# Kernel optimization log

Measured on AMD Instinct MI355X. Metric: run time of the kernel, lower is better.

## Reference

```python
import jax, jax.numpy as jnp
import numpy as np

NEG = -1e6  # masked_softmax fill value from the original code


def setup_inputs() -> dict:
    key = jax.random.key(0)
    ks = jax.random.split(key, 8)
    B, Q, K, Dq, Dk, Dv, H = 8, 256, 1024, 256, 256, 128, 128
    queries = jax.random.normal(ks[0], (B, Q, Dq), dtype=jnp.float32)
    keys = jax.random.normal(ks[1], (B, K, Dk), dtype=jnp.float32)
    values = jax.random.normal(ks[2], (B, K, Dv), dtype=jnp.float32)
    valid_lens = jax.random.randint(ks[3], (B,), 1, K + 1, dtype=jnp.int32)
    # learned params (Dense, use_bias=False): y = x @ W
    W_q = jax.random.normal(ks[4], (Dq, H), dtype=jnp.float32) / np.sqrt(Dq)
    W_k = jax.random.normal(ks[5], (Dk, H), dtype=jnp.float32) / np.sqrt(Dk)
    w_v = jax.random.normal(ks[6], (H,), dtype=jnp.float32) / np.sqrt(H)
    return {"queries": queries, "keys": keys, "values": values,
            "valid_lens": valid_lens, "W_q": W_q, "W_k": W_k, "w_v": w_v}


def reference(queries, keys, values, valid_lens, W_q, W_k, w_v):
    q = jnp.einsum('bqd,dh->bqh', queries, W_q)          # [B,Q,H]
    k = jnp.einsum('bkd,dh->bkh', keys, W_k)             # [B,K,H]
    features = jnp.tanh(q[:, :, None, :] + k[:, None, :, :])  # [B,Q,K,H]
    scores = jnp.einsum('bqkh,h->bqk', features, w_v)    # [B,Q,K]
    # masked softmax over last axis: positions >= valid_len set to -1e6
    K_len = scores.shape[-1]
    mask = jnp.arange(K_len)[None, None, :] < valid_lens[:, None, None]
    scores = jnp.where(mask, scores, NEG)
    attn = jax.nn.softmax(scores, axis=-1)
    return jnp.einsum('bqk,bkv->bqv', attn, values)      # [B,Q,Dv]
```

## Files before the change

kernel.cpp:

```cpp
#include <hip/hip_runtime.h>
#include <hip/hip_bf16.h>

#if defined(__has_builtin)
#if __has_builtin(__builtin_amdgcn_exp2f)
#define EXP2F __builtin_amdgcn_exp2f
#endif
#if __has_builtin(__builtin_amdgcn_rcpf)
#define RCPF __builtin_amdgcn_rcpf
#endif
#endif
#ifndef EXP2F
#define EXP2F exp2f
#endif
#ifndef RCPF
#define RCPF(x) (1.0f / (x))
#endif

#define B_  8
#define Q_  256
#define K_  1024
#define D_  256
#define H_  128
#define DV_ 128

#define CSL 2.8853900817779268f
#define L2E 1.4426950408889634f

#define QE_OFF   0
#define KE_OFF   262144
#define WPK_OFF  1310720
#define AVP_OFF  1310976
#define SP_OFF   1835264

__global__ __launch_bounds__(256) void proj_kernel(
    const float* __restrict__ queries, const float* __restrict__ keys,
    const float* __restrict__ Wq, const float* __restrict__ Wk,
    const float* __restrict__ w_v,
    float* __restrict__ qE, float2* __restrict__ kET2, float* __restrict__ wpk)
{
    __shared__ __align__(16) float As[64][68];
    __shared__ __align__(16) float Ws[64][64];

    const int tid = threadIdx.x;
    const int blk = blockIdx.x;
    const bool isQ = blk < 64;
    const int t = isQ ? blk : (blk - 64);
    const int rowtile = t >> 1;
    const int cbase = (t & 1) * 64;
    const int row0 = rowtile * 64;
    const float* A = isQ ? (queries + row0 * D_) : (keys + row0 * D_);
    const float* W = isQ ? Wq : Wk;

    float acc[4][4];
#pragma unroll
    for (int i = 0; i < 4; i++)
#pragma unroll
        for (int j = 0; j < 4; j++) acc[i][j] = 0.f;

    const int lr  = tid & 63;
    const int ldb = (tid >> 6) * 16;
    const int r4  = (tid >> 4) * 4;
    const int c4  = (tid & 15) * 4;

    for (int d0 = 0; d0 < D_; d0 += 64) {
#pragma unroll
        for (int j = 0; j < 4; j++) {
            const float4 a = *(const float4*)&A[lr * D_ + d0 + ldb + j * 4];
            As[ldb + j * 4 + 0][lr] = a.x;
            As[ldb + j * 4 + 1][lr] = a.y;
            As[ldb + j * 4 + 2][lr] = a.z;
            As[ldb + j * 4 + 3][lr] = a.w;
        }
#pragma unroll
        for (int l = 0; l < 4; l++) {
            const int idx = tid + l * 256;
            const int rr = idx >> 4, cc = (idx & 15) * 4;
            *(float4*)&Ws[rr][cc] = *(const float4*)&W[(d0 + rr) * H_ + cbase + cc];
        }
        __syncthreads();
#pragma unroll 4
        for (int d = 0; d < 64; d++) {
            const float4 a4 = *(const float4*)&As[d][r4];
            const float4 w4 = *(const float4*)&Ws[d][c4];
            const float ar[4] = {a4.x, a4.y, a4.z, a4.w};
#pragma unroll
            for (int i = 0; i < 4; i++) {
                acc[i][0] = fmaf(ar[i], w4.x, acc[i][0]);
                acc[i][1] = fmaf(ar[i], w4.y, acc[i][1]);
                acc[i][2] = fmaf(ar[i], w4.z, acc[i][2]);
                acc[i][3] = fmaf(ar[i], w4.w, acc[i][3]);
            }
        }
        __syncthreads();
    }

#pragma unroll
    for (int i = 0; i < 4; i++) {
        float e[4];
#pragma unroll
        for (int j = 0; j < 4; j++) e[j] = EXP2F(CSL * acc[i][j]);
        const int row = row0 + r4 + i;
        if (isQ) {
            *(float4*)&qE[row * H_ + cbase + c4] = make_float4(e[0], e[1], e[2], e[3]);
        } else {
            const int b = row >> 10, k = row & 1023;
            const int p0 = (cbase + c4) >> 1;
            kET2[(size_t)(b * 64 + p0) * K_ + k]     = make_float2(e[0], e[1]);
            kET2[(size_t)(b * 64 + p0 + 1) * K_ + k] = make_float2(e[2], e[3]);
        }
    }

    if (blk == 0 && tid < 64) {
        const float w1 = -2.0f * L2E * w_v[2 * tid];
        const float w2 = -2.0f * L2E * w_v[2 * tid + 1];
        *(float4*)&wpk[tid * 4] = make_float4(w1, w2, w1 + w2, 0.f);
    }
}

__global__ __launch_bounds__(512, 4) void attn_kernel(
    const float* __restrict__ qE,
    const float2* __restrict__ kET2,
    const float* __restrict__ values,
    const int*   __restrict__ valid_lens,
    const float* __restrict__ wpk,
    float* __restrict__ avpart,
    float* __restrict__ spart)
{
    __shared__ __align__(16) float sc[512][8];
    __shared__ __align__(16) float red[4][8][128];
    __shared__ __align__(16) float psum[8][8];

    const int tid = threadIdx.x;
    const int raw = blockIdx.x;
    const int kh  = raw >> 8;
    const int j   = raw & 255;
    const int b   = (j + kh) & 7;
    const int qt  = j >> 3;
    const int q0  = qt * 8;
    const int vl  = valid_lens[b];
    const int k   = kh * 512 + tid;

    const float* qp = qE + (b * Q_ + q0) * H_;

    float acc[8];
#pragma unroll
    for (int q = 0; q < 8; q++) acc[q] = 0.f;

    if (k < vl) {
        const float2* kb = kET2 + (size_t)(b * 64) * K_ + k;
#pragma unroll 2
        for (int p = 0; p < 64; p++) {
            const float2 ek = kb[(size_t)p * K_];
            const float4 wp = *(const float4*)&wpk[p * 4];
#pragma unroll
            for (int q = 0; q < 8; q++) {
                const float2 qq = *(const float2*)&qp[q * H_ + 2 * p];
                const float x1 = qq.x * ek.x, x2 = qq.y * ek.y;
                const float e1 = x1 + 1.f;
                const float d  = fmaf(e1, x2, e1);
                float n = fmaf(wp.y, x1, wp.z);
                n = fmaf(wp.x, x2, n);
                acc[q] = fmaf(n, RCPF(d), acc[q]);
            }
        }
    }

    const bool valid = k < vl;
    float p8[8];
#pragma unroll
    for (int q = 0; q < 8; q++) p8[q] = valid ? EXP2F(acc[q]) : 0.f;
    *(float4*)&sc[tid][0] = make_float4(p8[0], p8[1], p8[2], p8[3]);
    *(float4*)&sc[tid][4] = make_float4(p8[4], p8[5], p8[6], p8[7]);

    float s8[8];
#pragma unroll
    for (int q = 0; q < 8; q++) s8[q] = p8[q];
#pragma unroll
    for (int sh = 32; sh > 0; sh >>= 1) {
#pragma unroll
        for (int q = 0; q < 8; q++) s8[q] += __shfl_xor(s8[q], sh);
    }
    const int lane = tid & 63, w = tid >> 6;
    if (lane == 0) {
        *(float4*)&psum[w][0] = make_float4(s8[0], s8[1], s8[2], s8[3]);
        *(float4*)&psum[w][4] = make_float4(s8[4], s8[5], s8[6], s8[7]);
    }
    __syncthreads();
    if (tid < 8) {
        float t = 0.f;
#pragma unroll
        for (int ww = 0; ww < 8; ww++) t += psum[ww][tid];
        spart[kh * 2048 + b * Q_ + q0 + tid] = t;
    }

    const int v4  = tid & 31;
    const int qp2 = (tid >> 5) & 3;
    const int ks  = tid >> 7;
    const float* vb = values + (size_t)b * (K_ * DV_) + v4 * 4;
    float av[2][4];
#pragma unroll
    for (int qq = 0; qq < 2; qq++)
#pragma unroll
        for (int jj = 0; jj < 4; jj++) av[qq][jj] = 0.f;

    const int kbase = kh * 512 + ks * 128;
    const int rem = vl - kbase;
    const int imax = rem <= 0 ? 0 : (rem > 128 ? 128 : rem);
#pragma unroll 2
    for (int i = 0; i < imax; i++) {
        const int kl = ks * 128 + i;
        const float4 vv = *(const float4*)&vb[(kbase + i) * DV_];
        const float2 pp = *(const float2*)&sc[kl][2 * qp2];
        av[0][0] = fmaf(pp.x, vv.x, av[0][0]); av[0][1] = fmaf(pp.x, vv.y, av[0][1]);
        av[0][2] = fmaf(pp.x, vv.z, av[0][2]); av[0][3] = fmaf(pp.x, vv.w, av[0][3]);
        av[1][0] = fmaf(pp.y, vv.x, av[1][0]); av[1][1] = fmaf(pp.y, vv.y, av[1][1]);
        av[1][2] = fmaf(pp.y, vv.z, av[1][2]); av[1][3] = fmaf(pp.y, vv.w, av[1][3]);
    }
    *(float4*)&red[ks][2 * qp2][v4 * 4]     = make_float4(av[0][0], av[0][1], av[0][2], av[0][3]);
    *(float4*)&red[ks][2 * qp2 + 1][v4 * 4] = make_float4(av[1][0], av[1][1], av[1][2], av[1][3]);
    __syncthreads();

    if (tid < 256) {
        const int q = tid >> 5, vv4 = tid & 31;
        float4 t = make_float4(0.f, 0.f, 0.f, 0.f);
#pragma unroll
        for (int g = 0; g < 4; g++) {
            const float4 r = *(const float4*)&red[g][q][vv4 * 4];
            t.x += r.x; t.y += r.y; t.z += r.z; t.w += r.w;
        }
        *(float4*)&avpart[(size_t)(kh * 2048 + b * Q_ + q0 + q) * DV_ + vv4 * 4] = t;
    }
}

__global__ __launch_bounds__(256) void combine_kernel(
    const float* __restrict__ avpart, const float* __restrict__ spart,
    float* __restrict__ out)
{
    const int idx = (blockIdx.x * 256 + threadIdx.x) * 4;
    const int row = idx >> 7;
    const float4 a0 = *(const float4*)&avpart[idx];
    const float4 a1 = *(const float4*)&avpart[2048 * DV_ + idx];
    const float r = RCPF(spart[row] + spart[2048 + row]);
    *(float4*)&out[idx] = make_float4((a0.x + a1.x) * r, (a0.y + a1.y) * r,
                                      (a0.z + a1.z) * r, (a0.w + a1.w) * r);
}

extern "C" void kernel_launch(void* const* d_in, const int* in_sizes, int n_in,
                              void* d_out, int out_size, void* d_ws, size_t ws_size,
                              hipStream_t stream) {
    const float* queries    = (const float*)d_in[0];
    const float* keys       = (const float*)d_in[1];
    const float* values     = (const float*)d_in[2];
    const int*   valid_lens = (const int*)d_in[3];
    const float* W_q        = (const float*)d_in[4];
    const float* W_k        = (const float*)d_in[5];
    const float* w_v        = (const float*)d_in[6];
    float* out = (float*)d_out;

    float*  ws     = (float*)d_ws;
    float*  qE     = ws + QE_OFF;
    float2* kET2   = (float2*)(ws + KE_OFF);
    float*  wpk    = ws + WPK_OFF;
    float*  avpart = ws + AVP_OFF;
    float*  spart  = ws + SP_OFF;

    proj_kernel<<<320, 256, 0, stream>>>(queries, keys, W_q, W_k, w_v, qE, kET2, wpk);
    attn_kernel<<<512, 512, 0, stream>>>(qE, kET2, values, valid_lens, wpk, avpart, spart);
    combine_kernel<<<256, 256, 0, stream>>>(avpart, spart, out);
}
```

Baseline: 143.5 us.

## Split attention into 128-key chunks with early exit past valid length

The attention kernel is restructured from 512 blocks of 512 threads (two K halves, 8 queries) into 2048 blocks of 256 threads, each handling 8 queries over a 128-key chunk. Whole chunks beyond valid_len now exit immediately, which skips wasted work on padded keys and lets the grid balance across CUs with more, smaller blocks. The in-block AV reduction through shared memory is removed. In exchange the combine kernel sums up to 8 partials per row, and the partial buffers grow, so spart is moved to a new workspace offset.

```diff
diff --git a/kernel.cpp b/kernel.cpp
--- a/kernel.cpp
+++ b/kernel.cpp
@@ -30,7 +30,7 @@
 #define KE_OFF   262144
 #define WPK_OFF  1310720
 #define AVP_OFF  1310976
-#define SP_OFF   1835264
+#define SP_OFF   3408128
 
 __global__ __launch_bounds__(256) void proj_kernel(
     const float* __restrict__ queries, const float* __restrict__ keys,
@@ -117,7 +117,7 @@
     }
 }
 
-__global__ __launch_bounds__(512, 4) void attn_kernel(
+__global__ __launch_bounds__(256, 8) void attn_kernel(
     const float* __restrict__ qE,
     const float2* __restrict__ kET2,
     const float* __restrict__ values,
@@ -126,25 +126,25 @@
     float* __restrict__ avpart,
     float* __restrict__ spart)
 {
-    __shared__ __align__(16) float sc[512][8];
-    __shared__ __align__(16) float red[4][8][128];
-    __shared__ __align__(16) float psum[8][8];
+    __shared__ float sc[8][128];
+    __shared__ __align__(16) float psum[4][4];
 
     const int tid = threadIdx.x;
-    const int raw = blockIdx.x;
-    const int kh  = raw >> 8;
-    const int j   = raw & 255;
-    const int b   = (j + kh) & 7;
-    const int qt  = j >> 3;
-    const int q0  = qt * 8;
-    const int vl  = valid_lens[b];
-    const int k   = kh * 512 + tid;
-
-    const float* qp = qE + (b * Q_ + q0) * H_;
-
-    float acc[8];
-#pragma unroll
-    for (int q = 0; q < 8; q++) acc[q] = 0.f;
+    const int idx = blockIdx.x;
+    const int b  = idx & 7;
+    const int ks = (idx >> 3) & 7;
+    const int qt = idx >> 6;
+    const int vl = valid_lens[b];
+    const int k0 = ks * 128;
+    if (k0 >= vl) return;
+
+    const int q0 = qt * 8;
+    const int kl = tid & 127;
+    const int qh = tid >> 7;
+    const int k  = k0 + kl;
+    const float* qp = qE + (b * Q_ + q0 + qh * 4) * H_;
+
+    float acc[4] = {0.f, 0.f, 0.f, 0.f};
 
     if (k < vl) {
         const float2* kb = kET2 + (size_t)(b * 64) * K_ + k;
@@ -153,7 +153,7 @@
             const float2 ek = kb[(size_t)p * K_];
             const float4 wp = *(const float4*)&wpk[p * 4];
 #pragma unroll
-            for (int q = 0; q < 8; q++) {
+            for (int q = 0; q < 4; q++) {
                 const float2 qq = *(const float2*)&qp[q * H_ + 2 * p];
                 const float x1 = qq.x * ek.x, x2 = qq.y * ek.y;
                 const float e1 = x1 + 1.f;
@@ -166,83 +166,64 @@
     }
 
     const bool valid = k < vl;
-    float p8[8];
-#pragma unroll
-    for (int q = 0; q < 8; q++) p8[q] = valid ? EXP2F(acc[q]) : 0.f;
-    *(float4*)&sc[tid][0] = make_float4(p8[0], p8[1], p8[2], p8[3]);
-    *(float4*)&sc[tid][4] = make_float4(p8[4], p8[5], p8[6], p8[7]);
-
-    float s8[8];
-#pragma unroll
-    for (int q = 0; q < 8; q++) s8[q] = p8[q];
+    float p4[4];
+#pragma unroll
+    for (int q = 0; q < 4; q++) {
+        p4[q] = valid ? EXP2F(acc[q]) : 0.f;
+        sc[qh * 4 + q][kl] = p4[q];
+    }
 #pragma unroll
     for (int sh = 32; sh > 0; sh >>= 1) {
 #pragma unroll
-        for (int q = 0; q < 8; q++) s8[q] += __shfl_xor(s8[q], sh);
+        for (int q = 0; q < 4; q++) p4[q] += __shfl_xor(p4[q], sh);
     }
     const int lane = tid & 63, w = tid >> 6;
-    if (lane == 0) {
-        *(float4*)&psum[w][0] = make_float4(s8[0], s8[1], s8[2], s8[3]);
-        *(float4*)&psum[w][4] = make_float4(s8[4], s8[5], s8[6], s8[7]);
-    }
+    if (lane == 0) *(float4*)&psum[w][0] = make_float4(p4[0], p4[1], p4[2], p4[3]);
     __syncthreads();
     if (tid < 8) {
-        float t = 0.f;
-#pragma unroll
-        for (int ww = 0; ww < 8; ww++) t += psum[ww][tid];
-        spart[kh * 2048 + b * Q_ + q0 + tid] = t;
-    }
-
-    const int v4  = tid & 31;
-    const int qp2 = (tid >> 5) & 3;
-    const int ks  = tid >> 7;
-    const float* vb = values + (size_t)b * (K_ * DV_) + v4 * 4;
-    float av[2][4];
-#pragma unroll
-    for (int qq = 0; qq < 2; qq++)
-#pragma unroll
-        for (int jj = 0; jj < 4; jj++) av[qq][jj] = 0.f;
-
-    const int kbase = kh * 512 + ks * 128;
-    const int rem = vl - kbase;
-    const int imax = rem <= 0 ? 0 : (rem > 128 ? 128 : rem);
+        const int qh2 = tid >> 2, j = tid & 3;
+        spart[ks * 2048 + b * Q_ + q0 + tid] =
+            psum[2 * qh2][j] + psum[2 * qh2 + 1][j];
+    }
+
+    const int v4 = (tid & 31) * 4;
+    const int q  = tid >> 5;
+    const float* vb = values + (size_t)b * (K_ * DV_) + (size_t)k0 * DV_ + v4;
+    float av0 = 0.f, av1 = 0.f, av2 = 0.f, av3 = 0.f;
+    const int rem = vl - k0;
+    const int imax = rem > 128 ? 128 : rem;
 #pragma unroll 2
     for (int i = 0; i < imax; i++) {
-        const int kl = ks * 128 + i;
-        const float4 vv = *(const float4*)&vb[(kbase + i) * DV_];
-        const float2 pp = *(const float2*)&sc[kl][2 * qp2];
-        av[0][0] = fmaf(pp.x, vv.x, av[0][0]); av[0][1] = fmaf(pp.x, vv.y, av[0][1]);
-        av[0][2] = fmaf(pp.x, vv.z, av[0][2]); av[0][3] = fmaf(pp.x, vv.w, av[0][3]);
-        av[1][0] = fmaf(pp.y, vv.x, av[1][0]); av[1][1] = fmaf(pp.y, vv.y, av[1][1]);
-        av[1][2] = fmaf(pp.y, vv.z, av[1][2]); av[1][3] = fmaf(pp.y, vv.w, av[1][3]);
-    }
-    *(float4*)&red[ks][2 * qp2][v4 * 4]     = make_float4(av[0][0], av[0][1], av[0][2], av[0][3]);
-    *(float4*)&red[ks][2 * qp2 + 1][v4 * 4] = make_float4(av[1][0], av[1][1], av[1][2], av[1][3]);
-    __syncthreads();
-
-    if (tid < 256) {
-        const int q = tid >> 5, vv4 = tid & 31;
-        float4 t = make_float4(0.f, 0.f, 0.f, 0.f);
-#pragma unroll
-        for (int g = 0; g < 4; g++) {
-            const float4 r = *(const float4*)&red[g][q][vv4 * 4];
-            t.x += r.x; t.y += r.y; t.z += r.z; t.w += r.w;
-        }
-        *(float4*)&avpart[(size_t)(kh * 2048 + b * Q_ + q0 + q) * DV_ + vv4 * 4] = t;
-    }
+        const float4 vv = *(const float4*)&vb[i * DV_];
+        const float pp = sc[q][i];
+        av0 = fmaf(pp, vv.x, av0);
+        av1 = fmaf(pp, vv.y, av1);
+        av2 = fmaf(pp, vv.z, av2);
+        av3 = fmaf(pp, vv.w, av3);
+    }
+    *(float4*)&avpart[(size_t)(ks * 2048 + b * Q_ + q0 + q) * DV_ + v4] =
+        make_float4(av0, av1, av2, av3);
 }
 
 __global__ __launch_bounds__(256) void combine_kernel(
     const float* __restrict__ avpart, const float* __restrict__ spart,
-    float* __restrict__ out)
+    const int* __restrict__ valid_lens, float* __restrict__ out)
 {
-    const int idx = (blockIdx.x * 256 + threadIdx.x) * 4;
+    const int t = blockIdx.x * 256 + threadIdx.x;
+    const int idx = t * 4;
     const int row = idx >> 7;
-    const float4 a0 = *(const float4*)&avpart[idx];
-    const float4 a1 = *(const float4*)&avpart[2048 * DV_ + idx];
-    const float r = RCPF(spart[row] + spart[2048 + row]);
-    *(float4*)&out[idx] = make_float4((a0.x + a1.x) * r, (a0.y + a1.y) * r,
-                                      (a0.z + a1.z) * r, (a0.w + a1.w) * r);
+    const int b = row >> 8;
+    const int vl = valid_lens[b];
+    const int np = (vl + 127) >> 7;
+
+    float ax = 0.f, ay = 0.f, az = 0.f, aw = 0.f, s = 0.f;
+    for (int g = 0; g < np; g++) {
+        const float4 r = *(const float4*)&avpart[(size_t)g * 2048 * DV_ + idx];
+        ax += r.x; ay += r.y; az += r.z; aw += r.w;
+        s += spart[g * 2048 + row];
+    }
+    const float rr = RCPF(s);
+    *(float4*)&out[idx] = make_float4(ax * rr, ay * rr, az * rr, aw * rr);
 }
 
 extern "C" void kernel_launch(void* const* d_in, const int* in_sizes, int n_in,
@@ -265,6 +246,6 @@
     float*  spart  = ws + SP_OFF;
 
     proj_kernel<<<320, 256, 0, stream>>>(queries, keys, W_q, W_k, w_v, qE, kET2, wpk);
-    attn_kernel<<<512, 512, 0, stream>>>(qE, kET2, values, valid_lens, wpk, avpart, spart);
-    combine_kernel<<<256, 256, 0, stream>>>(avpart, spart, out);
-}
+    attn_kernel<<<2048, 256, 0, stream>>>(qE, kET2, values, valid_lens, wpk, avpart, spart);
+    combine_kernel<<<256, 256, 0, stream>>>(avpart, spart, valid_lens, out);
+}
```

After: 170.0 us. 1.18x slower.
